# Performance work log

Hardware: AMD Instinct MI355X
Metric: run time of the kernel (lower is better)

## Reference

```python
import jax, jax.numpy as jnp
from jax import lax
import numpy as np

B, N, CIN, COUT = 2, 4096, 64, 128
RADIUS = 0.15
K = int(16 * 1.5)
BN_EPS = 1e-5


def _conv1(x, w):  # 1x1 conv1d: x [B,C,N], w [O,C]
    return jnp.einsum('oc,bcn->bon', w, x)


def _conv2(x, w):  # 1x1 conv2d: x [B,C,N,K], w [O,C]
    return jnp.einsum('oc,bcnk->bonk', w, x)


def _bn(x, g, b):  # eval-mode BN with running_mean=0, running_var=1
    shp = (1, -1) + (1,) * (x.ndim - 2)
    scale = g / jnp.sqrt(1.0 + BN_EPS)
    return x * scale.reshape(shp) + b.reshape(shp)


def _ball_query(query, support, radius, k):
    # query [G,Q,3], support [G,S,3] -> idx [G,Q,k] (pointnet2 semantics:
    # first k in-radius support indices in order, padded with the first hit, 0 if none)
    q = lax.stop_gradient(query)
    s = lax.stop_gradient(support)
    d2 = (jnp.sum(q * q, -1)[:, :, None] + jnp.sum(s * s, -1)[:, None, :]
          - 2.0 * jnp.einsum('gqd,gsd->gqs', q, s))
    S = s.shape[1]
    score = jnp.where(d2 < radius * radius,
                      jnp.arange(S, dtype=jnp.int32)[None, None, :], jnp.int32(S))
    neg, idx = lax.top_k(-score, k)  # k smallest scores = first k hits
    valid = neg > -S
    first = jnp.where(valid[..., :1], idx[..., :1], 0)
    return jnp.where(valid, idx, first)


def _group(idx, support, query, feats):
    # support [G,S,3], query [G,Q,3], feats [G,C,S], idx [G,Q,k]
    gx = jax.vmap(lambda sp, ix: sp[ix])(support, idx)            # [G,Q,k,3]
    dp = jnp.transpose(gx - query[:, :, None, :], (0, 3, 1, 2))    # [G,3,Q,k]
    fj = jax.vmap(lambda fb, ix: fb[:, ix])(feats, idx)            # [G,C,Q,k]
    return dp, fj


def _fps_perm(pts):  # pts [K,3] -> FPS visiting order (permutation) [K] int32
    n = pts.shape[0]
    def step(carry, _):
        dists, last = carry
        d = jnp.sum((pts - pts[last]) ** 2, -1)
        dists = jnp.minimum(dists, d)
        nxt = jnp.argmax(dists).astype(jnp.int32)
        return (dists, nxt), nxt
    init = (jnp.full((n,), 1e10, pts.dtype), jnp.int32(0))
    _, rest = lax.scan(step, init, None, length=n - 1)
    return jnp.concatenate([jnp.zeros((1,), jnp.int32), rest])


def _forward(pc, f, pe_in, w1, g1, b1, wd1, gd1, bd1, wd2, gd2, bd2,
             wd3, gd3, bd3, ww, gw, bw, wc2, gc2, bc2):
    Bv, Nv, _ = pc.shape
    p = pc[..., :3]
    # convs1: conv1d + bn + relu
    f1 = jax.nn.relu(_bn(_conv1(f, w1), g1, b1))                   # [B,COUT,N]
    # main ball-query grouper (nsample=K)
    idx = _ball_query(p, p, RADIUS, K)                             # [B,N,K]
    dp, fj = _group(idx, p, p, f1)                                 # [B,3,N,K], [B,C,N,K]
    C = fj.shape[1]
    # torch .view(B*N, K, 3) on a contiguous [B,3,N,K] tensor (layout reinterpret,
    # replicated faithfully with reshape)
    new_dp = dp.reshape(Bv * Nv, K, 3)
    fidx = jax.vmap(_fps_perm)(lax.stop_gradient(new_dp))          # [B*N,K]
    new_dp = jnp.take_along_axis(new_dp, fidx[..., None], axis=1)
    new_dp = new_dp.reshape(Bv, 3, Nv, K)
    # deformable: 3->32->16->3, last block without activation
    h = jax.nn.relu(_bn(_conv2(new_dp, wd1), gd1, bd1))
    h = jax.nn.relu(_bn(_conv2(h, wd2), gd2, bd2))
    delta = _bn(_conv2(h, wd3), gd3, bd3)
    new_dp = new_dp + delta
    # np_assign: ball query with nsample=1 over each group of K points
    q2 = new_dp.reshape(Bv * Nv, K, 3)
    s2 = dp.reshape(Bv * Nv, K, 3)
    ft2 = fj.reshape(Bv * Nv, C, K)
    idx2 = _ball_query(q2, s2, RADIUS, 1)                          # [B*N,K,1]
    nn_dp, nn_fj = _group(idx2, s2, q2, ft2)                       # [B*N,3,K,1],[B*N,C,K,1]
    dp2 = nn_dp.reshape(Bv, 3, Nv, K)
    fj2 = nn_fj.reshape(Bv, C, Nv, K)
    # modulation weights + positional encoding
    mod = jax.nn.softmax(_bn(_conv2(fj2, ww), gw, bw), axis=-1)
    pe = jax.nn.relu(_bn(_conv2(dp2, wc2), gc2, bc2))
    fout = jnp.max((pe + fj2) * mod, axis=-1)                      # [B,COUT,N]
    return pc, fout, pe


def setup_inputs() -> dict:
    key = jax.random.key(0)
    ks = jax.random.split(key, 32)
    w = lambda k, o, i: jax.random.normal(k, (o, i), jnp.float32) * 0.05
    g = lambda k, c: jax.random.uniform(k, (c,), jnp.float32, 0.5, 1.5)
    b = lambda k, c: jax.random.normal(k, (c,), jnp.float32) * 0.05
    return {
        'pc': jax.random.uniform(ks[0], (B, N, 6), jnp.float32),
        'f': jax.random.normal(ks[1], (B, CIN, N), jnp.float32),
        'pe_in': jnp.zeros((B, 3, N), jnp.float32),
        'w1': w(ks[2], COUT, CIN), 'g1': g(ks[3], COUT), 'b1': b(ks[4], COUT),
        'wd1': w(ks[5], 32, 3), 'gd1': g(ks[6], 32), 'bd1': b(ks[7], 32),
        'wd2': w(ks[8], 16, 32), 'gd2': g(ks[9], 16), 'bd2': b(ks[10], 16),
        'wd3': w(ks[11], 3, 16), 'gd3': g(ks[12], 3), 'bd3': b(ks[13], 3),
        'ww': w(ks[14], COUT, COUT), 'gw': g(ks[15], COUT), 'bw': b(ks[16], COUT),
        'wc2': w(ks[17], COUT, 3), 'gc2': g(ks[18], COUT), 'bc2': b(ks[19], COUT),
    }


def reference(pc, f, pe_in, w1, g1, b1, wd1, gd1, bd1, wd2, gd2, bd2,
              wd3, gd3, bd3, ww, gw, bw, wc2, gc2, bc2):
    return _forward(pc, f, pe_in, w1, g1, b1, wd1, gd1, bd1, wd2, gd2, bd2,
                    wd3, gd3, bd3, ww, gw, bw, wc2, gc2, bc2)
```

## Files before the change

### kernel.cpp

```cpp
#include <hip/hip_runtime.h>
#include <stdint.h>


#define BB 2
#define NN 4096
#define CI 64
#define CO 128
#define KK 24
#define GQ (BB*NN)
#define NKK (NN*KK)

typedef __attribute__((ext_vector_type(8))) short short8;
typedef __attribute__((ext_vector_type(4))) float f32x4;

__device__ __forceinline__ float relu_(float x){ return fmaxf(x, 0.0f); }
__device__ __forceinline__ unsigned short f2bf(float x){
    unsigned int u = __float_as_uint(x);
    return (unsigned short)((u + 0x7FFFu + ((u>>16)&1u)) >> 16);
}

__global__ __launch_bounds__(256) void k_f1(const float* __restrict__ f, const float* __restrict__ w1,
                     const float* __restrict__ g1, const float* __restrict__ b1,
                     const float* __restrict__ pc, const float* __restrict__ ww,
                     float* __restrict__ f1T, float* __restrict__ outPc,
                     float* __restrict__ p, float* __restrict__ pS,
                     unsigned short* __restrict__ wwAbf)
{
    int tid = threadIdx.x;
    int bid = blockIdx.x;
    {
        int t = bid*256 + tid;
        if (t < BB*NN*6) {
            float v = pc[t];
            outPc[t] = v;
            int d = t % 6;
            if (d < 3) {
                int q = t/6;
                p[q*3 + d] = v;
                pS[d*GQ + q] = v;
            }
        }
        if (t < CO*CO) {
            int o = t >> 7, c = t & 127;
            int otile = o >> 4, m = o & 15;
            int ks = c >> 5, kk = c & 31;
            int lane = m | ((kk >> 3) << 4);
            int j = kk & 7;
            wwAbf[(((otile*4 + ks)*64 + lane)<<3) + j] = f2bf(ww[t]);
        }
    }
    __shared__ float W[CI*129];
    __shared__ float ft[CI*16];
    for (int i = tid; i < CI*CO; i += 256) {
        int o = i >> 6, c = i & 63;
        W[c*129 + o] = w1[i];
    }
    int b = bid >> 8;
    int n0 = (bid & 255) * 16;
    {
        int c = tid >> 2, nn = (tid & 3) * 4;
        float4 v = *(const float4*)(f + (size_t)b*CI*NN + (size_t)c*NN + n0 + nn);
        *(float4*)&ft[c*16 + nn] = v;
    }
    __syncthreads();
    int o = tid & 127, g = tid >> 7;
    float acc[8];
    #pragma unroll
    for (int j = 0; j < 8; ++j) acc[j] = 0.f;
    const float* ftg = ft + g*8;
    #pragma unroll 8
    for (int c = 0; c < CI; ++c) {
        float w = W[c*129 + o];
        float4 fa = *(const float4*)&ftg[c*16];
        float4 fb4 = *(const float4*)&ftg[c*16 + 4];
        acc[0] += w*fa.x;  acc[1] += w*fa.y;  acc[2] += w*fa.z;  acc[3] += w*fa.w;
        acc[4] += w*fb4.x; acc[5] += w*fb4.y; acc[6] += w*fb4.z; acc[7] += w*fb4.w;
    }
    float sc = g1[o] / sqrtf(1.00001f);
    float bo = b1[o];
    #pragma unroll
    for (int j = 0; j < 8; ++j) {
        int n = n0 + g*8 + j;
        f1T[((size_t)b*NN + n)*CO + o] = relu_(acc[j]*sc + bo);
    }
}

__global__ __launch_bounds__(512) void k_bq1(const float* __restrict__ pS, int* __restrict__ idx)
{
    __shared__ float L[3*NN];
    int tid = threadIdx.x;
    int wave = tid >> 6;
    int lane = tid & 63;
    int q = blockIdx.x*8 + wave;
    int b = q >> 12;
    int n = q & 4095;
    int boff = b << 12;
    for (int i = tid; i < 3*(NN/4); i += 512) {
        int d = i >> 10, e = i & 1023;
        float4 v = *(const float4*)(pS + (size_t)d*GQ + boff + e*4);
        *(float4*)&L[d*NN + e*4] = v;
    }
    __syncthreads();
    const float* Lx = L;
    const float* Ly = L + NN;
    const float* Lz = L + 2*NN;
    float qx = Lx[n], qy = Ly[n], qz = Lz[n];
    float sq = qx*qx + qy*qy + qz*qz;
    const float rsq = (float)(0.15*0.15);
    int cnt = 0, first = 0;
    int* orow = idx + (size_t)q*KK;
    for (int chunk = 0; chunk < 64; ++chunk) {
        int s = chunk*64 + lane;
        float sx = Lx[s], sy = Ly[s], sz = Lz[s];
        float ss  = sx*sx + sy*sy + sz*sz;
        float dot = qx*sx + qy*sy + qz*sz;
        float d2 = (sq + ss) - 2.0f*dot;
        unsigned long long m = __ballot(d2 < rsq);
        while (m && cnt < KK) {
            int pos = __ffsll((unsigned long long)m) - 1;
            int sidx = chunk*64 + pos;
            if (cnt == 0) first = sidx;
            if (lane == 0) orow[cnt] = sidx;
            ++cnt;
            m &= m - 1;
        }
        if (cnt >= KK) break;
    }
    if (lane == 0)
        for (int j = cnt; j < KK; ++j) orow[j] = first;
}

__global__ __launch_bounds__(256) void k_geo(const float* __restrict__ p, const int* __restrict__ idx,
                                             float* __restrict__ dpf, float* __restrict__ ndp)
{
    int tid = threadIdx.x;
    int lane = tid & 31;
    int row = blockIdx.x*8 + (tid >> 5);
    float px = 0.f, py = 0.f, pz = 0.f, dist;
    if (lane < KK) {
        float v[3];
        #pragma unroll
        for (int d = 0; d < 3; ++d) {
            int u = 3*lane + d;
            int qq = u / 24;
            int kk = u - qq*24;
            int m = row*3 + qq;
            int b = (m >= 3*NN) ? 1 : 0;
            int rem = m - b*3*NN;
            int dd = rem >> 12;
            int n = rem & 4095;
            int base = (b << 12);
            int j = idx[((size_t)(base + n))*KK + kk];
            v[d] = p[(base + j)*3 + dd] - p[(base + n)*3 + dd];
        }
        px = v[0]; py = v[1]; pz = v[2];
        dist = 1e10f;
        float* drow = dpf + (size_t)row*72 + lane*3;
        drow[0] = px; drow[1] = py; drow[2] = pz;
    } else {
        dist = -3.4e38f;
    }
    float* dst = ndp + (size_t)row*72;
    if (lane == 0) { dst[0] = px; dst[1] = py; dst[2] = pz; }
    int last = 0;
    for (int j = 1; j < KK; ++j) {
        float lx = __shfl(px, last, 32);
        float ly = __shfl(py, last, 32);
        float lz = __shfl(pz, last, 32);
        float dx = px-lx, dy = py-ly, dz = pz-lz;
        float d = dx*dx + dy*dy + dz*dz;
        dist = fminf(dist, d);
        float val = dist; int idxl = lane;
        #pragma unroll
        for (int off = 16; off > 0; off >>= 1) {
            float ov = __shfl_xor(val, off, 32);
            int   oi = __shfl_xor(idxl, off, 32);
            if (ov > val || (ov == val && oi < idxl)) { val = ov; idxl = oi; }
        }
        if (lane == idxl) { dst[j*3+0] = px; dst[j*3+1] = py; dst[j*3+2] = pz; }
        last = idxl;
    }
}

__global__ void k_mlp(const float* __restrict__ ndp,
                      const float* __restrict__ wd1, const float* __restrict__ gd1, const float* __restrict__ bd1,
                      const float* __restrict__ wd2, const float* __restrict__ gd2, const float* __restrict__ bd2,
                      const float* __restrict__ wd3, const float* __restrict__ gd3, const float* __restrict__ bd3,
                      float* __restrict__ q2)
{
    __shared__ float W1[96], S1[32], B1s[32], W2[512], S2[16], B2s[16], W3[48], S3[3], B3s[3];
    int tid = threadIdx.x;
    const float inv = sqrtf(1.00001f);
    for (int i = tid; i < 96;  i += blockDim.x) W1[i]=wd1[i];
    for (int i = tid; i < 512; i += blockDim.x) W2[i]=wd2[i];
    for (int i = tid; i < 48;  i += blockDim.x) W3[i]=wd3[i];
    if (tid < 32) { S1[tid]=gd1[tid]/inv; B1s[tid]=bd1[tid]; }
    if (tid >= 32 && tid < 48) { int c=tid-32; S2[c]=gd2[c]/inv; B2s[c]=bd2[c]; }
    if (tid >= 48 && tid < 51) { int c=tid-48; S3[c]=gd3[c]/inv; B3s[c]=bd3[c]; }
    __syncthreads();
    int t = blockIdx.x*blockDim.x + tid;
    int k = t % KK, n = (t/KK)%NN, b = t/(NN*KK);
    size_t base = (((size_t)b*3)*NN + n)*KK + k;
    float x0 = ndp[base], x1 = ndp[base + NKK], x2 = ndp[base + 2*(size_t)NKK];
    float h1[32];
    #pragma unroll
    for (int o = 0; o < 32; ++o)
        h1[o] = relu_((W1[o*3+0]*x0 + W1[o*3+1]*x1 + W1[o*3+2]*x2)*S1[o] + B1s[o]);
    float h2[16];
    #pragma unroll
    for (int o = 0; o < 16; ++o) {
        float a = 0.f;
        #pragma unroll
        for (int c = 0; c < 32; ++c) a += W2[o*32+c]*h1[c];
        h2[o] = relu_(a*S2[o] + B2s[o]);
    }
    float xv[3] = {x0, x1, x2};
    #pragma unroll
    for (int d = 0; d < 3; ++d) {
        float a = 0.f;
        #pragma unroll
        for (int c = 0; c < 16; ++c) a += W3[d*16+c]*h2[c];
        q2[base + (size_t)d*NKK] = xv[d] + (a*S3[d] + B3s[d]);
    }
}

__global__ void k_bq2(const float* __restrict__ dpf, const float* __restrict__ q2f,
                      int* __restrict__ idx2, float* __restrict__ dp2)
{
    int t = blockIdx.x*blockDim.x + threadIdx.x;
    int g = t / KK, kq = t % KK;
    const float* srow = dpf + (size_t)g*72;
    const float* qp   = q2f + (size_t)g*72 + kq*3;
    float qx=qp[0], qy=qp[1], qz=qp[2];
    float sq = qx*qx + qy*qy + qz*qz;
    const float rsq = (float)(0.15*0.15);
    int j2 = 0;
    for (int s = 0; s < KK; ++s) {
        float sx=srow[s*3+0], sy=srow[s*3+1], sz=srow[s*3+2];
        float ss  = sx*sx + sy*sy + sz*sz;
        float dot = qx*sx + qy*sy + qz*sz;
        float d2 = (sq + ss) - 2.0f*dot;
        if (d2 < rsq) { j2 = s; break; }
    }
    idx2[t] = j2;
    float* drow = dp2 + (size_t)g*72;
    drow[0*KK + kq] = srow[j2*3+0] - qx;
    drow[1*KK + kq] = srow[j2*3+1] - qy;
    drow[2*KK + kq] = srow[j2*3+2] - qz;
}

__global__ __launch_bounds__(256, 4) void k_final(
    const float* __restrict__ f1T, const int* __restrict__ idx, const int* __restrict__ idx2,
    const float* __restrict__ dp2, const unsigned short* __restrict__ wwAbf,
    const float* __restrict__ gw, const float* __restrict__ bw,
    const float* __restrict__ wc2, const float* __restrict__ gc2, const float* __restrict__ bc2,
    float* __restrict__ fout, float* __restrict__ pe)
{
    __shared__ float GM[6400];
    __shared__ unsigned short Fbf[48*128];
    __shared__ float Ds[2][3][KK];
    int tid = threadIdx.x;
    int bid0 = blockIdx.x;
    int bid = ((bid0 & 7) << 9) | (bid0 >> 3);
    int b = bid >> 11;
    int n0 = (bid & 2047)*2;

    if (tid >= 64 && tid < 208) {
        int u = tid-64; int nl = u/72, r = u%72, d = r/24, k = r%24;
        Ds[nl][d][k] = dp2[(((size_t)b*3 + d)*NN + (n0+nl))*KK + k];
    }
    int c = tid & 127, kh = tid >> 7;
    int khs = __builtin_amdgcn_readfirstlane(kh);
    int4 irA0, irA1, irA2, irB0, irB1, irB2;
    {
        const int4* r0 = (const int4*)(idx + ((size_t)b*NN + n0)*KK + khs*12);
        const int4* r1 = (const int4*)(idx + ((size_t)b*NN + n0+1)*KK + khs*12);
        irA0 = r0[0]; irA1 = r0[1]; irA2 = r0[2];
        irB0 = r1[0]; irB1 = r1[1]; irB2 = r1[2];
    }
    int i2r[12];
    {
        int g = (b*CO + c)*32 + (n0 >> 7);
        const int4* i4 = (const int4*)(idx2 + (size_t)g*KK) + kh*3;
        int4 a = i4[0], bq = i4[1], cq4 = i4[2];
        i2r[0]=a.x; i2r[1]=a.y; i2r[2]=a.z; i2r[3]=a.w;
        i2r[4]=bq.x; i2r[5]=bq.y; i2r[6]=bq.z; i2r[7]=bq.w;
        i2r[8]=cq4.x; i2r[9]=cq4.y; i2r[10]=cq4.z; i2r[11]=cq4.w;
    }
    int wv = tid >> 6, l = tid & 63;
    const short8* wwA8 = (const short8*)wwAbf;
    short8 Af[2][4];
    #pragma unroll
    for (int ot = 0; ot < 2; ++ot)
        #pragma unroll
        for (int ks = 0; ks < 4; ++ks)
            Af[ot][ks] = wwA8[((wv*2 + ot)*4 + ks)*64 + l];

    const float* basep = f1T + (size_t)b*NN*CO + c;
    {
        int irv[2][12] = {{irA0.x,irA0.y,irA0.z,irA0.w, irA1.x,irA1.y,irA1.z,irA1.w, irA2.x,irA2.y,irA2.z,irA2.w},
                          {irB0.x,irB0.y,irB0.z,irB0.w, irB1.x,irB1.y,irB1.z,irB1.w, irB2.x,irB2.y,irB2.z,irB2.w}};
        #pragma unroll
        for (int nl = 0; nl < 2; ++nl)
            #pragma unroll
            for (int j = 0; j < 12; ++j) {
                int kk = khs*12 + j;
                GM[nl*3200 + c*25 + kk] = basep[(size_t)irv[nl][j]*CO];
            }
    }
    __syncthreads();

    #pragma unroll
    for (int nl = 0; nl < 2; ++nl)
        #pragma unroll
        for (int j = 0; j < 12; ++j) {
            int col = nl*24 + kh*12 + j;
            unsigned int boff = (unsigned)((col*256 + c*2) ^ ((col&7)<<4));
            *(unsigned short*)((char*)Fbf + boff) = f2bf(GM[nl*3200 + c*25 + i2r[j]]);
        }
    __syncthreads();

    {
        f32x4 acc[2][3];
        #pragma unroll
        for (int ot=0;ot<2;++ot)
            #pragma unroll
            for (int ct=0;ct<3;++ct)
                acc[ot][ct] = (f32x4){0.f,0.f,0.f,0.f};
        int row_l = l & 15, kc_l = (l >> 4) << 3;
        #pragma unroll
        for (int ct = 0; ct < 3; ++ct) {
            int row = ct*16 + row_l;
            #pragma unroll
            for (int ks = 0; ks < 4; ++ks) {
                unsigned int boff = (unsigned)((row*256 + (ks*32 + kc_l)*2) ^ ((row&7)<<4));
                short8 Bf = *(const short8*)((const char*)Fbf + boff);
                acc[0][ct] = __builtin_amdgcn_mfma_f32_16x16x32_bf16(Af[0][ks], Bf, acc[0][ct], 0,0,0);
                acc[1][ct] = __builtin_amdgcn_mfma_f32_16x16x32_bf16(Af[1][ks], Bf, acc[1][ct], 0,0,0);
            }
        }
        #pragma unroll
        for (int ot = 0; ot < 2; ++ot) {
            int o = wv*32 + ot*16 + ((l>>4)<<2);
            #pragma unroll
            for (int ct = 0; ct < 3; ++ct) {
                int col = ct*16 + (l & 15);
                *(f32x4*)&GM[col*132 + o] = acc[ot][ct];
            }
        }
    }
    __syncthreads();

    int op = (tid & 127) >> 1, half = tid & 1, nl = tid >> 7;
    int k0 = half*12;
    int o0 = op*2;
    int n  = n0 + nl;
    int colb = nl*24 + k0;
    float a0[12], a1[12];
    #pragma unroll
    for (int j = 0; j < 12; ++j) {
        float2 m2 = *(const float2*)&GM[(colb+j)*132 + o0];
        a0[j] = m2.x; a1[j] = m2.y;
    }
    const float inv = sqrtf(1.00001f);
    float sw0 = gw[o0]/inv,   bw0 = bw[o0];
    float sw1 = gw[o0+1]/inv, bw1 = bw[o0+1];
    float pev0[12], pev1[12];
    {
        float wa0=wc2[o0*3], wa1=wc2[o0*3+1], wa2=wc2[o0*3+2];
        float wb0=wc2[o0*3+3], wb1=wc2[o0*3+4], wb2=wc2[o0*3+5];
        float sca = gc2[o0]/inv,   bca = bc2[o0];
        float scb = gc2[o0+1]/inv, bcb = bc2[o0+1];
        #pragma unroll
        for (int j = 0; j < 12; ++j) {
            float d0 = Ds[nl][0][k0+j], d1 = Ds[nl][1][k0+j], d2 = Ds[nl][2][k0+j];
            pev0[j] = relu_((wa0*d0 + wa1*d1 + wa2*d2)*sca + bca);
            pev1[j] = relu_((wb0*d0 + wb1*d1 + wb2*d2)*scb + bcb);
        }
    }
    float m0 = -3.4e38f, m1 = -3.4e38f;
    #pragma unroll
    for (int j=0;j<12;++j){
        a0[j] = a0[j]*sw0 + bw0; m0 = fmaxf(m0, a0[j]);
        a1[j] = a1[j]*sw1 + bw1; m1 = fmaxf(m1, a1[j]);
    }
    m0 = fmaxf(m0, __shfl_xor(m0, 1));
    m1 = fmaxf(m1, __shfl_xor(m1, 1));
    float s0 = 0.f, s1 = 0.f;
    #pragma unroll
    for (int j=0;j<12;++j){
        a0[j] = __expf(a0[j]-m0); s0 += a0[j];
        a1[j] = __expf(a1[j]-m1); s1 += a1[j];
    }
    s0 += __shfl_xor(s0, 1);
    s1 += __shfl_xor(s1, 1);
    float rs0 = 1.0f/s0, rs1 = 1.0f/s1;
    float fo0 = -3.4e38f, fo1 = -3.4e38f;
    #pragma unroll
    for (int j=0;j<12;++j){
        unsigned int boff = (unsigned)(((colb+j)*256 + o0*2) ^ (((colb+j)&7)<<4));
        unsigned int v = *(const unsigned int*)((const char*)Fbf + boff);
        float fj0 = __uint_as_float((v & 0xffffu) << 16);
        float fj1 = __uint_as_float((v >> 16) << 16);
        fo0 = fmaxf(fo0, (pev0[j] + fj0)*a0[j]*rs0);
        fo1 = fmaxf(fo1, (pev1[j] + fj1)*a1[j]*rs1);
    }
    fo0 = fmaxf(fo0, __shfl_xor(fo0, 1));
    fo1 = fmaxf(fo1, __shfl_xor(fo1, 1));
    fout[((size_t)b*CO + o0+half)*NN + n] = half ? fo1 : fo0;
    float* pr0 = pe + (((size_t)b*CO + o0)*NN + n)*KK + k0;
    float* pr1 = pe + (((size_t)b*CO + o0+1)*NN + n)*KK + k0;
    #pragma unroll
    for (int q4 = 0; q4 < 3; ++q4) {
        float4 v0, v1;
        v0.x=pev0[q4*4+0]; v0.y=pev0[q4*4+1]; v0.z=pev0[q4*4+2]; v0.w=pev0[q4*4+3];
        v1.x=pev1[q4*4+0]; v1.y=pev1[q4*4+1]; v1.z=pev1[q4*4+2]; v1.w=pev1[q4*4+3];
        ((float4*)pr0)[q4] = v0;
        ((float4*)pr1)[q4] = v1;
    }
}

extern "C" void kernel_launch(void* const* d_in, const int* in_sizes, int n_in,
                              void* d_out, int out_size, void* d_ws, size_t ws_size,
                              hipStream_t stream)
{
    const float* pc  = (const float*)d_in[0];
    const float* f   = (const float*)d_in[1];
    const float* w1  = (const float*)d_in[3];
    const float* g1  = (const float*)d_in[4];
    const float* b1  = (const float*)d_in[5];
    const float* wd1 = (const float*)d_in[6];
    const float* gd1 = (const float*)d_in[7];
    const float* bd1 = (const float*)d_in[8];
    const float* wd2 = (const float*)d_in[9];
    const float* gd2 = (const float*)d_in[10];
    const float* bd2 = (const float*)d_in[11];
    const float* wd3 = (const float*)d_in[12];
    const float* gd3 = (const float*)d_in[13];
    const float* bd3 = (const float*)d_in[14];
    const float* ww  = (const float*)d_in[15];
    const float* gw  = (const float*)d_in[16];
    const float* bw  = (const float*)d_in[17];
    const float* wc2 = (const float*)d_in[18];
    const float* gc2 = (const float*)d_in[19];
    const float* bc2 = (const float*)d_in[20];

    float* out     = (float*)d_out;
    float* outPc   = out;
    float* outFout = out + 49152;
    float* outPe   = out + 49152 + 1048576;

    char* ws = (char*)d_ws;
    size_t off = 0;
    auto alloc = [&](size_t bytes)->void* {
        void* q = ws + off; off += (bytes + 255) & ~(size_t)255; return q;
    };
    float* p    = (float*)alloc((size_t)GQ*3*4);
    float* pS   = (float*)alloc((size_t)GQ*3*4);
    float* f1T  = (float*)alloc((size_t)BB*NN*CO*4);
    int*   idx  = (int*)  alloc((size_t)BB*NN*KK*4);
    float* dpf  = (float*)alloc((size_t)BB*3*NN*KK*4);
    float* ndp  = (float*)alloc((size_t)BB*3*NN*KK*4);
    float* q2f  = (float*)alloc((size_t)BB*3*NN*KK*4);
    int*   idx2 = (int*)  alloc((size_t)GQ*KK*4);
    float* dp2  = (float*)alloc((size_t)GQ*72*4);
    unsigned short* wwAbf = (unsigned short*)alloc((size_t)CO*CO*2);

    k_f1   <<<dim3(512), dim3(256), 0, stream>>>(f, w1, g1, b1, pc, ww, f1T, outPc, p, pS, wwAbf);
    k_bq1  <<<dim3(GQ/8), dim3(512), 0, stream>>>(pS, idx);
    k_geo  <<<dim3(GQ/8), dim3(256), 0, stream>>>(p, idx, dpf, ndp);
    k_mlp  <<<dim3((BB*NN*KK)/256), dim3(256), 0, stream>>>(ndp, wd1,gd1,bd1, wd2,gd2,bd2, wd3,gd3,bd3, q2f);
    k_bq2  <<<dim3((GQ*KK)/256), dim3(256), 0, stream>>>(dpf, q2f, idx2, dp2);
    k_final<<<dim3(BB*NN/2), dim3(256), 0, stream>>>(f1T, idx, idx2, dp2, wwAbf, gw, bw, wc2, gc2, bc2, outFout, outPe);
}
```

Measured before the change: 122.6 us.

## Fuse displacement MLP into second ball query and shrink k_final shared memory to bf16

```diff
diff --git a/kernel.cpp b/kernel.cpp
--- a/kernel.cpp
+++ b/kernel.cpp
@@ -17,6 +17,9 @@
 __device__ __forceinline__ unsigned short f2bf(float x){
     unsigned int u = __float_as_uint(x);
     return (unsigned short)((u + 0x7FFFu + ((u>>16)&1u)) >> 16);
+}
+__device__ __forceinline__ float bf2f(unsigned int bits){
+    return __uint_as_float(bits << 16);
 }
 
 __global__ __launch_bounds__(256) void k_f1(const float* __restrict__ f, const float* __restrict__ w1,
@@ -182,11 +185,11 @@
     }
 }
 
-__global__ void k_mlp(const float* __restrict__ ndp,
+__global__ __launch_bounds__(256) void k_disp(const float* __restrict__ dpf, const float* __restrict__ ndp,
                       const float* __restrict__ wd1, const float* __restrict__ gd1, const float* __restrict__ bd1,
                       const float* __restrict__ wd2, const float* __restrict__ gd2, const float* __restrict__ bd2,
                       const float* __restrict__ wd3, const float* __restrict__ gd3, const float* __restrict__ bd3,
-                      float* __restrict__ q2)
+                      int* __restrict__ idx2, float* __restrict__ dp2)
 {
     __shared__ float W1[96], S1[32], B1s[32], W2[512], S2[16], B2s[16], W3[48], S3[3], B3s[3];
     int tid = threadIdx.x;
@@ -199,39 +202,39 @@
     if (tid >= 48 && tid < 51) { int c=tid-48; S3[c]=gd3[c]/inv; B3s[c]=bd3[c]; }
     __syncthreads();
     int t = blockIdx.x*blockDim.x + tid;
-    int k = t % KK, n = (t/KK)%NN, b = t/(NN*KK);
-    size_t base = (((size_t)b*3)*NN + n)*KK + k;
-    float x0 = ndp[base], x1 = ndp[base + NKK], x2 = ndp[base + 2*(size_t)NKK];
-    float h1[32];
-    #pragma unroll
-    for (int o = 0; o < 32; ++o)
-        h1[o] = relu_((W1[o*3+0]*x0 + W1[o*3+1]*x1 + W1[o*3+2]*x2)*S1[o] + B1s[o]);
-    float h2[16];
-    #pragma unroll
-    for (int o = 0; o < 16; ++o) {
+    int g = t / KK, kq = t % KK;
+
+    float qc[3];
+    #pragma unroll
+    for (int e = 0; e < 3; ++e) {
+        int flat = 72*g + 3*kq + e;
+        int b = flat / (3*NKK);
+        int rem = flat - b*(3*NKK);
+        int d = rem / NKK;
+        int nk = rem - d*NKK;
+        const float* nb = ndp + (size_t)b*(3*NKK) + nk;
+        float x0 = nb[0], x1 = nb[NKK], x2 = nb[2*NKK];
+        float h1[32];
+        #pragma unroll
+        for (int o = 0; o < 32; ++o)
+            h1[o] = relu_((W1[o*3+0]*x0 + W1[o*3+1]*x1 + W1[o*3+2]*x2)*S1[o] + B1s[o]);
+        float h2[16];
+        #pragma unroll
+        for (int o = 0; o < 16; ++o) {
+            float a = 0.f;
+            #pragma unroll
+            for (int c = 0; c < 32; ++c) a += W2[o*32+c]*h1[c];
+            h2[o] = relu_(a*S2[o] + B2s[o]);
+        }
         float a = 0.f;
         #pragma unroll
-        for (int c = 0; c < 32; ++c) a += W2[o*32+c]*h1[c];
-        h2[o] = relu_(a*S2[o] + B2s[o]);
-    }
-    float xv[3] = {x0, x1, x2};
-    #pragma unroll
-    for (int d = 0; d < 3; ++d) {
-        float a = 0.f;
-        #pragma unroll
         for (int c = 0; c < 16; ++c) a += W3[d*16+c]*h2[c];
-        q2[base + (size_t)d*NKK] = xv[d] + (a*S3[d] + B3s[d]);
-    }
-}
-
-__global__ void k_bq2(const float* __restrict__ dpf, const float* __restrict__ q2f,
-                      int* __restrict__ idx2, float* __restrict__ dp2)
-{
-    int t = blockIdx.x*blockDim.x + threadIdx.x;
-    int g = t / KK, kq = t % KK;
+        float xd = (d==0) ? x0 : ((d==1) ? x1 : x2);
+        qc[e] = xd + (a*S3[d] + B3s[d]);
+    }
+
     const float* srow = dpf + (size_t)g*72;
-    const float* qp   = q2f + (size_t)g*72 + kq*3;
-    float qx=qp[0], qy=qp[1], qz=qp[2];
+    float qx=qc[0], qy=qc[1], qz=qc[2];
     float sq = qx*qx + qy*qy + qz*qz;
     const float rsq = (float)(0.15*0.15);
     int j2 = 0;
@@ -249,14 +252,14 @@
     drow[2*KK + kq] = srow[j2*3+2] - qz;
 }
 
-__global__ __launch_bounds__(256, 4) void k_final(
+__global__ __launch_bounds__(256, 6) void k_final(
     const float* __restrict__ f1T, const int* __restrict__ idx, const int* __restrict__ idx2,
     const float* __restrict__ dp2, const unsigned short* __restrict__ wwAbf,
     const float* __restrict__ gw, const float* __restrict__ bw,
     const float* __restrict__ wc2, const float* __restrict__ gc2, const float* __restrict__ bc2,
     float* __restrict__ fout, float* __restrict__ pe)
 {
-    __shared__ float GM[6400];
+    __shared__ unsigned short GsM[2*128*26];
     __shared__ unsigned short Fbf[48*128];
     __shared__ float Ds[2][3][KK];
     int tid = threadIdx.x;
@@ -305,7 +308,7 @@
             #pragma unroll
             for (int j = 0; j < 12; ++j) {
                 int kk = khs*12 + j;
-                GM[nl*3200 + c*25 + kk] = basep[(size_t)irv[nl][j]*CO];
+                GsM[nl*3328 + c*26 + kk] = f2bf(basep[(size_t)irv[nl][j]*CO]);
             }
     }
     __syncthreads();
@@ -316,7 +319,7 @@
         for (int j = 0; j < 12; ++j) {
             int col = nl*24 + kh*12 + j;
             unsigned int boff = (unsigned)((col*256 + c*2) ^ ((col&7)<<4));
-            *(unsigned short*)((char*)Fbf + boff) = f2bf(GM[nl*3200 + c*25 + i2r[j]]);
+            *(unsigned short*)((char*)Fbf + boff) = GsM[nl*3328 + c*26 + i2r[j]];
         }
     __syncthreads();
 
@@ -345,7 +348,11 @@
             #pragma unroll
             for (int ct = 0; ct < 3; ++ct) {
                 int col = ct*16 + (l & 15);
-                *(f32x4*)&GM[col*132 + o] = acc[ot][ct];
+                f32x4 a = acc[ot][ct];
+                uint2 pk;
+                pk.x = (unsigned)f2bf(a[0]) | ((unsigned)f2bf(a[1]) << 16);
+                pk.y = (unsigned)f2bf(a[2]) | ((unsigned)f2bf(a[3]) << 16);
+                *(uint2*)&GsM[col*132 + o] = pk;
             }
         }
     }
@@ -359,8 +366,9 @@
     float a0[12], a1[12];
     #pragma unroll
     for (int j = 0; j < 12; ++j) {
-        float2 m2 = *(const float2*)&GM[(colb+j)*132 + o0];
-        a0[j] = m2.x; a1[j] = m2.y;
+        unsigned int v = *(const unsigned int*)&GsM[(colb+j)*132 + o0];
+        a0[j] = bf2f(v & 0xffffu);
+        a1[j] = bf2f(v >> 16);
     }
     const float inv = sqrtf(1.00001f);
     float sw0 = gw[o0]/inv,   bw0 = bw[o0];
@@ -400,8 +408,8 @@
     for (int j=0;j<12;++j){
         unsigned int boff = (unsigned)(((colb+j)*256 + o0*2) ^ (((colb+j)&7)<<4));
         unsigned int v = *(const unsigned int*)((const char*)Fbf + boff);
-        float fj0 = __uint_as_float((v & 0xffffu) << 16);
-        float fj1 = __uint_as_float((v >> 16) << 16);
+        float fj0 = bf2f(v & 0xffffu);
+        float fj1 = bf2f(v >> 16);
         fo0 = fmaxf(fo0, (pev0[j] + fj0)*a0[j]*rs0);
         fo1 = fmaxf(fo1, (pev1[j] + fj1)*a1[j]*rs1);
     }
@@ -461,7 +469,6 @@
     int*   idx  = (int*)  alloc((size_t)BB*NN*KK*4);
     float* dpf  = (float*)alloc((size_t)BB*3*NN*KK*4);
     float* ndp  = (float*)alloc((size_t)BB*3*NN*KK*4);
-    float* q2f  = (float*)alloc((size_t)BB*3*NN*KK*4);
     int*   idx2 = (int*)  alloc((size_t)GQ*KK*4);
     float* dp2  = (float*)alloc((size_t)GQ*72*4);
     unsigned short* wwAbf = (unsigned short*)alloc((size_t)CO*CO*2);
@@ -469,7 +476,6 @@
     k_f1   <<<dim3(512), dim3(256), 0, stream>>>(f, w1, g1, b1, pc, ww, f1T, outPc, p, pS, wwAbf);
     k_bq1  <<<dim3(GQ/8), dim3(512), 0, stream>>>(pS, idx);
     k_geo  <<<dim3(GQ/8), dim3(256), 0, stream>>>(p, idx, dpf, ndp);
-    k_mlp  <<<dim3((BB*NN*KK)/256), dim3(256), 0, stream>>>(ndp, wd1,gd1,bd1, wd2,gd2,bd2, wd3,gd3,bd3, q2f);
-    k_bq2  <<<dim3((GQ*KK)/256), dim3(256), 0, stream>>>(dpf, q2f, idx2, dp2);
+    k_disp <<<dim3((GQ*KK)/256), dim3(256), 0, stream>>>(dpf, ndp, wd1,gd1,bd1, wd2,gd2,bd2, wd3,gd3,bd3, idx2, dp2);
     k_final<<<dim3(BB*NN/2), dim3(256), 0, stream>>>(f1T, idx, idx2, dp2, wwAbf, gw, bw, wc2, gc2, bc2, outFout, outPe);
 }
```

New measurement: 151.5 us. +23.6%, slower.
